# Optimization experiments

Measured on AMD Instinct MI355X. Metric: run time of the kernel, lower is better.

## Reference

```python
import jax, jax.numpy as jnp
import numpy as np
import math

EMB_DIM = 1024
NUM_HEADS = 16
D_H = EMB_DIM // NUM_HEADS
B, S = 2, 2048


def setup_inputs() -> dict:
    key = jax.random.key(0)
    ks = jax.random.split(key, 6)
    limit = math.sqrt(6.0 / (EMB_DIM + D_H))  # xavier_uniform per head
    x = jax.random.normal(ks[0], (B, S, EMB_DIM), dtype=jnp.float32)
    Wq = jax.random.uniform(ks[1], (NUM_HEADS, EMB_DIM, D_H), jnp.float32, -limit, limit)
    Wk = jax.random.uniform(ks[2], (NUM_HEADS, EMB_DIM, D_H), jnp.float32, -limit, limit)
    Wv = jax.random.uniform(ks[3], (NUM_HEADS, EMB_DIM, D_H), jnp.float32, -limit, limit)
    bq = jnp.zeros((NUM_HEADS, D_H), jnp.float32)
    bk = jnp.zeros((NUM_HEADS, D_H), jnp.float32)
    bv = jnp.zeros((NUM_HEADS, D_H), jnp.float32)
    limo = math.sqrt(6.0 / (EMB_DIM + EMB_DIM))
    W_O = jax.random.uniform(ks[4], (EMB_DIM, EMB_DIM), jnp.float32, -limo, limo)
    causal_mask = jnp.tril(jnp.ones((S, S), jnp.float32))
    padding_mask = jnp.zeros((B, S), jnp.bool_)  # all-False: nothing padded
    return {"x": x, "Wq": Wq, "bq": bq, "Wk": Wk, "bk": bk, "Wv": Wv,
            "bv": bv, "W_O": W_O, "causal_mask": causal_mask,
            "padding_mask": padding_mask}


def reference(x, Wq, bq, Wk, bk, Wv, bv, W_O, causal_mask, padding_mask):
    # Per-head projections, vectorized over heads: [B,S,E] x [H,E,D] -> [B,H,S,D]
    Q = jnp.einsum('bse,hed->bhsd', x, Wq) + bq[None, :, None, :]
    K = jnp.einsum('bse,hed->bhsd', x, Wk) + bk[None, :, None, :]
    V = jnp.einsum('bse,hed->bhsd', x, Wv) + bv[None, :, None, :]
    scores = jnp.einsum('bhsd,bhtd->bhst', Q, K) / math.sqrt(D_H)
    neg_inf = jnp.float32(-jnp.inf)
    scores = jnp.where(causal_mask[None, None, :, :] == 0, neg_inf, scores)
    scores = jnp.where(padding_mask[:, None, None, :], neg_inf, scores)
    attn = jax.nn.softmax(scores, axis=-1)
    out = jnp.einsum('bhst,bhtd->bhsd', attn, V)  # [B,H,S,D]
    # concat heads in order (dim=-1) -> [B,S,H*D]
    x_concat = out.transpose(0, 2, 1, 3).reshape(B, S, EMB_DIM)
    return x_concat @ W_O
```

## Files before the change

### kernel.cpp

```cpp
#include <hip/hip_runtime.h>
#include <hip/hip_bf16.h>


typedef __hip_bfloat16 bf16;
typedef __attribute__((ext_vector_type(8))) short bfrag;
typedef __attribute__((ext_vector_type(4))) float f32x4;
typedef __attribute__((ext_vector_type(16))) float f32x16;
typedef __attribute__((ext_vector_type(4))) short short4v;

#define MFMA16(a, b, c) __builtin_amdgcn_mfma_f32_16x16x32_bf16(a, b, c, 0, 0, 0)
#define MFMA32(a, b, c) __builtin_amdgcn_mfma_f32_32x32x16_bf16(a, b, c, 0, 0, 0)

__global__ __launch_bounds__(256) void prep_all(const float* __restrict__ x,
                                                const float* __restrict__ Wq,
                                                const float* __restrict__ Wk,
                                                const float* __restrict__ Wv,
                                                const float* __restrict__ Wo,
                                                bf16* __restrict__ xb,
                                                bf16* __restrict__ WqkvT,
                                                bf16* __restrict__ WoT) {
  __shared__ bf16 tile[64][80];
  int id = blockIdx.x;
  int t = threadIdx.x;
  if (id < 2048) {
    int i = id * 2048 + t * 8;
    float4 a = *(const float4*)(x + i);
    float4 b = *(const float4*)(x + i + 4);
    union { bf16 h[8]; bfrag v; } tmp;
    tmp.h[0] = __float2bfloat16(a.x); tmp.h[1] = __float2bfloat16(a.y);
    tmp.h[2] = __float2bfloat16(a.z); tmp.h[3] = __float2bfloat16(a.w);
    tmp.h[4] = __float2bfloat16(b.x); tmp.h[5] = __float2bfloat16(b.y);
    tmp.h[6] = __float2bfloat16(b.z); tmp.h[7] = __float2bfloat16(b.w);
    *(bfrag*)(xb + i) = tmp.v;
    return;
  }
  int wid = id - 2048;
  const float* src;
  bf16* dst;
  int srcld, dstld, r0, c0;
  if (wid < 768) {
    int w = wid >> 8, h = (wid >> 4) & 15;
    r0 = (wid & 15) * 64; c0 = 0;
    src = ((w == 0) ? Wq : (w == 1) ? Wk : Wv) + (long)h * 1024 * 64;
    dst = WqkvT + ((long)w * 1024 + h * 64) * 1024;
    srcld = 64; dstld = 1024;
  } else {
    int j = wid - 768;
    c0 = (j & 15) * 64; r0 = (j >> 4) * 64;
    src = Wo; dst = WoT;
    srcld = 1024; dstld = 1024;
  }
  int lr = t >> 3, lc = (t & 7) << 3;
#pragma unroll
  for (int p = 0; p < 2; ++p) {
    int r = lr + p * 32;
    const float* s = src + (long)(r0 + r) * srcld + c0 + lc;
    union { bf16 h8[8]; bfrag v; } tmp;
#pragma unroll
    for (int j = 0; j < 8; ++j) tmp.h8[j] = __float2bfloat16(s[j]);
    *(bfrag*)(&tile[r][lc]) = tmp.v;
  }
  __syncthreads();
#pragma unroll
  for (int p = 0; p < 2; ++p) {
    int c = lr + p * 32;
    union { bf16 h8[8]; bfrag v; } tmp;
#pragma unroll
    for (int j = 0; j < 8; ++j) tmp.h8[j] = tile[lc + j][c];
    *(bfrag*)(dst + (long)(c0 + c) * dstld + r0 + lc) = tmp.v;
  }
}

__global__ __launch_bounds__(256) void gemm_qkv128(const bf16* __restrict__ xb,
                                                   const bf16* __restrict__ WT,
                                                   const float* __restrict__ bq,
                                                   const float* __restrict__ bk,
                                                   const float* __restrict__ bv,
                                                   bf16* __restrict__ Q,
                                                   bf16* __restrict__ K_,
                                                   bf16* __restrict__ Vt) {
  const int K = 1024;
  __shared__ bf16 As[128][72];
  __shared__ bf16 Bs[128][72];
  int id = blockIdx.x;
  int xcd = id & 7, s = id >> 3;
  int m0 = ((xcd << 2) | (s & 3)) * 128;
  int n0 = (s >> 2) * 128;
  int t = threadIdx.x, wave = t >> 6, lane = t & 63, quad = lane >> 4, col = lane & 15;
  int wr = (wave >> 1) * 64, wc = (wave & 1) * 64;
  f32x4 acc[4][4] = {};

  int srow = t >> 1, scol = (t & 1) * 32;
  const bf16* Ag = xb + (long)(m0 + srow) * K + scol;
  const bf16* Bg = WT + (long)(n0 + srow) * K + scol;

  bfrag A0[4], B0[4], A1[4], B1[4];
#pragma unroll
  for (int i = 0; i < 4; ++i) {
    A0[i] = *(const bfrag*)(Ag + 8 * i);
    B0[i] = *(const bfrag*)(Bg + 8 * i);
    A1[i] = *(const bfrag*)(Ag + 64 + 8 * i);
    B1[i] = *(const bfrag*)(Bg + 64 + 8 * i);
  }

  for (int k0 = 0; k0 < K; k0 += 64) {
    __syncthreads();
#pragma unroll
    for (int i = 0; i < 4; ++i) {
      *(bfrag*)(&As[srow][scol + 8 * i]) = A0[i];
      *(bfrag*)(&Bs[srow][scol + 8 * i]) = B0[i];
    }
    int kn = (k0 + 128 < K) ? k0 + 128 : K - 64;
#pragma unroll
    for (int i = 0; i < 4; ++i) {
      A0[i] = A1[i]; B0[i] = B1[i];
      A1[i] = *(const bfrag*)(Ag + kn + 8 * i);
      B1[i] = *(const bfrag*)(Bg + kn + 8 * i);
    }
    __syncthreads();
#pragma unroll
    for (int kc = 0; kc < 2; ++kc) {
      bfrag ra[4], rb[4];
#pragma unroll
      for (int i = 0; i < 4; ++i)
        ra[i] = *(const bfrag*)(&As[wr + 16 * i + col][kc * 32 + quad * 8]);
#pragma unroll
      for (int c = 0; c < 4; ++c)
        rb[c] = *(const bfrag*)(&Bs[wc + 16 * c + col][kc * 32 + quad * 8]);
#pragma unroll
      for (int c = 0; c < 4; ++c)
#pragma unroll
        for (int i = 0; i < 4; ++i) acc[c][i] = MFMA16(ra[i], rb[c], acc[c][i]);
    }
  }

  int sel = n0 >> 10;
  const float* bias = (sel == 0) ? bq : (sel == 1) ? bk : bv;
#pragma unroll
  for (int c = 0; c < 4; ++c) {
    int nn = (n0 + wc + 16 * c + col) & 1023;
    float bvv = bias[nn];
    int h = nn >> 6, d = nn & 63;
#pragma unroll
    for (int i = 0; i < 4; ++i) {
      int mb = m0 + wr + 16 * i + quad * 4;
      int b = mb >> 11, s0 = mb & 2047;
      if (sel < 2) {
        bf16* dst = (sel == 0) ? Q : K_;
        long base = ((long)((b << 4) + h) * 2048 + s0) * 64 + d;
#pragma unroll
        for (int r = 0; r < 4; ++r)
          dst[base + (long)r * 64] = __float2bfloat16(acc[c][i][r] + bvv);
      } else {
        union { bf16 h4[4]; short4v v; } pk;
#pragma unroll
        for (int r = 0; r < 4; ++r) pk.h4[r] = __float2bfloat16(acc[c][i][r] + bvv);
        *(short4v*)(Vt + (long)(((b << 4) + h) * 64 + d) * 2048 + s0) = pk.v;
      }
    }
  }
}

__global__ __launch_bounds__(256) void gemm_out(const bf16* __restrict__ O,
                                                const bf16* __restrict__ Bt,
                                                float* __restrict__ Cf) {
  const int K = 1024;
  __shared__ bf16 As[128][72];
  __shared__ bf16 Bs[64][72];
  int id = blockIdx.x;
  int xcd = id & 7, s = id >> 3;
  int m0 = ((xcd << 2) | (s & 3)) * 128;
  int n0 = (s >> 2) * 64;
  int t = threadIdx.x;
  int wave = t >> 6, lane = t & 63, quad = lane >> 4, col = lane & 15;
  int wr = (wave >> 1) * 64, wc = (wave & 1) * 32;
  f32x4 acc[2][4] = {};

  int srA = t >> 1, scA = (t & 1) * 32;
  int srB = t >> 2, scB = (t & 3) * 16;
  int mrow = m0 + srA;
  int ob = mrow >> 11, os = mrow & 2047;
  const bf16* Ag = O + (long)ob * 2097152 + (long)os * 64 + scA;
  const bf16* Bg = Bt + (long)(n0 + srB) * K + scB;

  bfrag A0[4], A1[4];
  bfrag B0[2], B1[2];
#pragma unroll
  for (int i = 0; i < 4; ++i) {
    A0[i] = *(const bfrag*)(Ag + 8 * i);
    A1[i] = *(const bfrag*)(Ag + (long)64 * 2048 + 8 * i);
  }
#pragma unroll
  for (int i = 0; i < 2; ++i) {
    B0[i] = *(const bfrag*)(Bg + 8 * i);
    B1[i] = *(const bfrag*)(Bg + 64 + 8 * i);
  }

  for (int k0 = 0; k0 < K; k0 += 64) {
    __syncthreads();
#pragma unroll
    for (int i = 0; i < 4; ++i) *(bfrag*)(&As[srA][scA + 8 * i]) = A0[i];
#pragma unroll
    for (int i = 0; i < 2; ++i) *(bfrag*)(&Bs[srB][scB + 8 * i]) = B0[i];
    int kn = (k0 + 128 < K) ? k0 + 128 : K - 64;
#pragma unroll
    for (int i = 0; i < 4; ++i) {
      A0[i] = A1[i];
      A1[i] = *(const bfrag*)(Ag + (long)kn * 2048 + 8 * i);
    }
#pragma unroll
    for (int i = 0; i < 2; ++i) {
      B0[i] = B1[i];
      B1[i] = *(const bfrag*)(Bg + kn + 8 * i);
    }
    __syncthreads();
#pragma unroll
    for (int kc = 0; kc < 2; ++kc) {
      bfrag ra[4], rb[2];
#pragma unroll
      for (int i = 0; i < 4; ++i)
        ra[i] = *(const bfrag*)(&As[wr + 16 * i + col][kc * 32 + quad * 8]);
#pragma unroll
      for (int c = 0; c < 2; ++c)
        rb[c] = *(const bfrag*)(&Bs[wc + 16 * c + col][kc * 32 + quad * 8]);
#pragma unroll
      for (int c = 0; c < 2; ++c)
#pragma unroll
        for (int i = 0; i < 4; ++i) acc[c][i] = MFMA16(ra[i], rb[c], acc[c][i]);
    }
  }

#pragma unroll
  for (int c = 0; c < 2; ++c) {
    int n = n0 + wc + 16 * c + col;
#pragma unroll
    for (int i = 0; i < 4; ++i)
#pragma unroll
      for (int r = 0; r < 4; ++r) {
        int m = m0 + wr + 16 * i + quad * 4 + r;
        Cf[(long)m * 1024 + n] = acc[c][i][r];
      }
  }
}

__global__ __launch_bounds__(256) void attn_kernel(const bf16* __restrict__ Q,
                                                   const bf16* __restrict__ K_,
                                                   const bf16* __restrict__ Vt,
                                                   bf16* __restrict__ O) {
  int id = blockIdx.x;
  int xcd = id & 7, kk = id >> 3;
  int bh = ((kk & 3) << 3) | xcd;
  int pair = kk >> 2;

  __shared__ bf16 Ks[128][72];
  __shared__ bf16 Vs[64][136];
  __shared__ bf16 Ps[64][136];

  int t = threadIdx.x, wave = t >> 6, lane = t & 63;
  int qh = wave >> 1, jh = wave & 1, hi = lane >> 5, l5 = lane & 31;

  const float SC2 = 0.18033688f;

  int krow = t >> 3, kg = (t & 7) * 8;
  int vrow = t >> 4, vg = (t & 15) * 8;
  const bf16* Kbase = K_ + ((long)bh * 2048 + krow) * 64 + kg;
  const bf16* Vbase = Vt + ((long)bh * 64 + vrow) * 2048 + vg;

#pragma unroll
  for (int qsel = 0; qsel < 2; ++qsel) {
    int qt = qsel ? (31 - pair) : pair;
    int q0 = qt * 64;
    int nj = (qt >> 1) + 1;

    bfrag qa[4];
    const bf16* qp = Q + ((long)bh * 2048 + q0 + 32 * qh + l5) * 64 + hi * 8;
#pragma unroll
    for (int kd = 0; kd < 4; ++kd) qa[kd] = *(const bfrag*)(qp + kd * 16);

    f32x16 o0, o1;
    float lsum[16];
#pragma unroll
    for (int r = 0; r < 16; ++r) { o0[r] = 0.f; o1[r] = 0.f; lsum[r] = 0.f; }

    bfrag kreg[4], vreg[4];
#pragma unroll
    for (int i = 0; i < 4; ++i)
      kreg[i] = *(const bfrag*)(Kbase + (long)(32 * i) * 64);

    for (int jt = 0; jt < nj; ++jt) {
      int j0 = jt * 128;
      __syncthreads();
#pragma unroll
      for (int i = 0; i < 4; ++i)
        *(bfrag*)(&Ks[krow + 32 * i][kg]) = kreg[i];
      int jn = (jt + 1 < nj) ? (jt + 1) * 128 : jt * 128;
#pragma unroll
      for (int i = 0; i < 4; ++i)
        vreg[i] = *(const bfrag*)(Vbase + (long)(16 * i) * 2048 + j0);
#pragma unroll
      for (int i = 0; i < 4; ++i)
        kreg[i] = *(const bfrag*)(Kbase + (long)(jn + 32 * i) * 64);
      __syncthreads();

      f32x16 s0, s1;
#pragma unroll
      for (int r = 0; r < 16; ++r) { s0[r] = 0.f; s1[r] = 0.f; }
#pragma unroll
      for (int kd = 0; kd < 4; ++kd) {
        bfrag kb0 = *(const bfrag*)(&Ks[jh * 64 + l5][kd * 16 + hi * 8]);
        bfrag kb1 = *(const bfrag*)(&Ks[jh * 64 + 32 + l5][kd * 16 + hi * 8]);
        s0 = MFMA32(qa[kd], kb0, s0);
        s1 = MFMA32(qa[kd], kb1, s1);
      }

      bool lastT = (jt == nj - 1);
#pragma unroll
      for (int jb = 0; jb < 2; ++jb) {
        int j = j0 + jh * 64 + jb * 32 + l5;
#pragma unroll
        for (int r = 0; r < 16; ++r) {
          int qrow = (r & 3) + 8 * (r >> 2) + 4 * hi;
          float sv = jb ? s1[r] : s0[r];
          float p = __builtin_amdgcn_exp2f(fmaf(sv, SC2, -16.0f));
          if (lastT) p = (j <= q0 + 32 * qh + qrow) ? p : 0.f;
          lsum[r] += p;
          Ps[32 * qh + qrow][jh * 64 + jb * 32 + l5] = __float2bfloat16(p);
        }
      }
#pragma unroll
      for (int i = 0; i < 4; ++i)
        *(bfrag*)(&Vs[vrow + 16 * i][vg]) = vreg[i];
      __syncthreads();

#pragma unroll
      for (int kj = 0; kj < 4; ++kj) {
        bfrag pa = *(const bfrag*)(&Ps[32 * qh + l5][jh * 64 + kj * 16 + hi * 8]);
        bfrag vb0 = *(const bfrag*)(&Vs[l5][jh * 64 + kj * 16 + hi * 8]);
        bfrag vb1 = *(const bfrag*)(&Vs[32 + l5][jh * 64 + kj * 16 + hi * 8]);
        o0 = MFMA32(pa, vb0, o0);
        o1 = MFMA32(pa, vb1, o1);
      }
    }

#pragma unroll
    for (int off = 1; off < 32; off <<= 1)
#pragma unroll
      for (int r = 0; r < 16; ++r) lsum[r] += __shfl_xor(lsum[r], off, 64);

    __syncthreads();
    float* Osc = (float*)&Ps[0][0];
    float* Lsc = (float*)&Vs[0][0];
    if (jh == 1) {
#pragma unroll
      for (int r = 0; r < 16; ++r) {
        int qrow = (r & 3) + 8 * (r >> 2) + 4 * hi;
        Osc[(qh * 32 + qrow) * 68 + 0 * 32 + l5] = o0[r];
        Osc[(qh * 32 + qrow) * 68 + 1 * 32 + l5] = o1[r];
      }
      if (l5 == 0) {
#pragma unroll
        for (int r = 0; r < 16; ++r) {
          int qrow = (r & 3) + 8 * (r >> 2) + 4 * hi;
          Lsc[qh * 32 + qrow] = lsum[r];
        }
      }
    }
    __syncthreads();
    if (jh == 0) {
#pragma unroll
      for (int r = 0; r < 16; ++r) {
        int qrow = (r & 3) + 8 * (r >> 2) + 4 * hi;
        float inv = 1.f / (lsum[r] + Lsc[qh * 32 + qrow]);
        int iq = q0 + 32 * qh + qrow;
        float v0 = o0[r] + Osc[(qh * 32 + qrow) * 68 + 0 * 32 + l5];
        float v1 = o1[r] + Osc[(qh * 32 + qrow) * 68 + 1 * 32 + l5];
        O[((long)bh * 2048 + iq) * 64 + l5] = __float2bfloat16(v0 * inv);
        O[((long)bh * 2048 + iq) * 64 + 32 + l5] = __float2bfloat16(v1 * inv);
      }
    }
  }
}

extern "C" void kernel_launch(void* const* d_in, const int* in_sizes, int n_in,
                              void* d_out, int out_size, void* d_ws, size_t ws_size,
                              hipStream_t stream) {
  const float* x  = (const float*)d_in[0];
  const float* Wq = (const float*)d_in[1];
  const float* bq = (const float*)d_in[2];
  const float* Wk = (const float*)d_in[3];
  const float* bk = (const float*)d_in[4];
  const float* Wv = (const float*)d_in[5];
  const float* bv = (const float*)d_in[6];
  const float* Wo = (const float*)d_in[7];
  float* out = (float*)d_out;

  bf16* ws = (bf16*)d_ws;
  const long MB1 = 1 << 20;
  bf16* WqkvT = ws + 0 * MB1;
  bf16* WoT   = ws + 3 * MB1;
  bf16* Q     = ws + 4 * MB1;
  bf16* K_    = ws + 8 * MB1;
  bf16* Vt    = ws + 12 * MB1;
  bf16* O     = ws + 16 * MB1;
  bf16* xb    = ws + 20 * MB1;

  prep_all<<<3072, 256, 0, stream>>>(x, Wq, Wk, Wv, Wo, xb, WqkvT, WoT);
  gemm_qkv128<<<768, 256, 0, stream>>>(xb, WqkvT, bq, bk, bv, Q, K_, Vt);
  attn_kernel<<<512, 256, 0, stream>>>(Q, K_, Vt, O);
  gemm_out<<<512, 256, 0, stream>>>(O, WoT, out);
}
```

Measured before the change: 211.2 us.

## Stage GEMM epilogues through LDS for coalesced stores; split attention into per-tile blocks

The QKV and output GEMM epilogues now write accumulators into shared memory first and then store full 16-byte rows to global memory, replacing scattered 2-byte and 4-byte stores. The attention kernel no longer pairs a short and a long query tile inside each block. It launches 1024 blocks, one query tile each, ordered longest first. This is meant to cut uncoalesced write traffic and give the scheduler more, finer-grained work, at the cost of extra barriers and LDS round trips and less balanced per-block work.

```diff
diff --git a/kernel.cpp b/kernel.cpp
--- a/kernel.cpp
+++ b/kernel.cpp
@@ -80,12 +80,13 @@
                                                    bf16* __restrict__ K_,
                                                    bf16* __restrict__ Vt) {
   const int K = 1024;
-  __shared__ bf16 As[128][72];
-  __shared__ bf16 Bs[128][72];
+  __shared__ __align__(16) bf16 SH[2 * 128 * 72];
+#define AS(r, c) SH[(r) * 72 + (c)]
+#define BS(r, c) SH[9216 + (r) * 72 + (c)]
   int id = blockIdx.x;
-  int xcd = id & 7, s = id >> 3;
-  int m0 = ((xcd << 2) | (s & 3)) * 128;
-  int n0 = (s >> 2) * 128;
+  int xcd = id & 7, sw = id >> 3;
+  int m0 = ((xcd << 2) | (sw & 3)) * 128;
+  int n0 = (sw >> 2) * 128;
   int t = threadIdx.x, wave = t >> 6, lane = t & 63, quad = lane >> 4, col = lane & 15;
   int wr = (wave >> 1) * 64, wc = (wave & 1) * 64;
   f32x4 acc[4][4] = {};
@@ -107,8 +108,8 @@
     __syncthreads();
 #pragma unroll
     for (int i = 0; i < 4; ++i) {
-      *(bfrag*)(&As[srow][scol + 8 * i]) = A0[i];
-      *(bfrag*)(&Bs[srow][scol + 8 * i]) = B0[i];
+      *(bfrag*)(&AS(srow, scol + 8 * i)) = A0[i];
+      *(bfrag*)(&BS(srow, scol + 8 * i)) = B0[i];
     }
     int kn = (k0 + 128 < K) ? k0 + 128 : K - 64;
 #pragma unroll
@@ -123,10 +124,10 @@
       bfrag ra[4], rb[4];
 #pragma unroll
       for (int i = 0; i < 4; ++i)
-        ra[i] = *(const bfrag*)(&As[wr + 16 * i + col][kc * 32 + quad * 8]);
+        ra[i] = *(const bfrag*)(&AS(wr + 16 * i + col, kc * 32 + quad * 8));
 #pragma unroll
       for (int c = 0; c < 4; ++c)
-        rb[c] = *(const bfrag*)(&Bs[wc + 16 * c + col][kc * 32 + quad * 8]);
+        rb[c] = *(const bfrag*)(&BS(wc + 16 * c + col, kc * 32 + quad * 8));
 #pragma unroll
       for (int c = 0; c < 4; ++c)
 #pragma unroll
@@ -136,41 +137,68 @@
 
   int sel = n0 >> 10;
   const float* bias = (sel == 0) ? bq : (sel == 1) ? bk : bv;
-#pragma unroll
-  for (int c = 0; c < 4; ++c) {
-    int nn = (n0 + wc + 16 * c + col) & 1023;
-    float bvv = bias[nn];
-    int h = nn >> 6, d = nn & 63;
-#pragma unroll
-    for (int i = 0; i < 4; ++i) {
-      int mb = m0 + wr + 16 * i + quad * 4;
-      int b = mb >> 11, s0 = mb & 2047;
-      if (sel < 2) {
-        bf16* dst = (sel == 0) ? Q : K_;
-        long base = ((long)((b << 4) + h) * 2048 + s0) * 64 + d;
+  int blk_b = m0 >> 11, blk_s = m0 & 2047;
+  __syncthreads();
+
+  if (sel < 2) {
+#pragma unroll
+    for (int c = 0; c < 4; ++c) {
+      int nl = wc + 16 * c + col;
+      float bvv = bias[(n0 + nl) & 1023];
+#pragma unroll
+      for (int i = 0; i < 4; ++i) {
+        int mb = wr + 16 * i + quad * 4;
 #pragma unroll
         for (int r = 0; r < 4; ++r)
-          dst[base + (long)r * 64] = __float2bfloat16(acc[c][i][r] + bvv);
-      } else {
+          SH[(mb + r) * 136 + nl] = __float2bfloat16(acc[c][i][r] + bvv);
+      }
+    }
+    __syncthreads();
+    int m = t >> 1, half = t & 1;
+    int h = (((n0 & 1023) >> 6) + half);
+    bf16* dst = (sel == 0) ? Q : K_;
+    bf16* p = dst + (((long)(blk_b * 16 + h)) * 2048 + blk_s + m) * 64;
+#pragma unroll
+    for (int j = 0; j < 8; ++j)
+      *(bfrag*)(p + 8 * j) = *(const bfrag*)(&SH[m * 136 + half * 64 + 8 * j]);
+  } else {
+#pragma unroll
+    for (int c = 0; c < 4; ++c) {
+      int nl = wc + 16 * c + col;
+      float bvv = bias[(n0 + nl) & 1023];
+#pragma unroll
+      for (int i = 0; i < 4; ++i) {
+        int mb = wr + 16 * i + quad * 4;
         union { bf16 h4[4]; short4v v; } pk;
 #pragma unroll
         for (int r = 0; r < 4; ++r) pk.h4[r] = __float2bfloat16(acc[c][i][r] + bvv);
-        *(short4v*)(Vt + (long)(((b << 4) + h) * 64 + d) * 2048 + s0) = pk.v;
+        *(short4v*)(&SH[nl * 136 + mb]) = pk.v;
       }
     }
-  }
+    __syncthreads();
+    int nl = t >> 1, mhalf = (t & 1) * 64;
+    int h = ((n0 & 1023) + nl) >> 6, d = nl & 63;
+    bf16* p = Vt + ((long)(blk_b * 16 + h) * 64 + d) * 2048 + blk_s + mhalf;
+#pragma unroll
+    for (int j = 0; j < 8; ++j)
+      *(bfrag*)(p + 8 * j) = *(const bfrag*)(&SH[nl * 136 + mhalf + 8 * j]);
+  }
+#undef AS
+#undef BS
 }
 
 __global__ __launch_bounds__(256) void gemm_out(const bf16* __restrict__ O,
                                                 const bf16* __restrict__ Bt,
                                                 float* __restrict__ Cf) {
   const int K = 1024;
-  __shared__ bf16 As[128][72];
-  __shared__ bf16 Bs[64][72];
+  __shared__ __align__(16) char SHB[34816];
+  bf16* SH = (bf16*)SHB;
+#define AS(r, c) SH[(r) * 72 + (c)]
+#define BS(r, c) SH[9216 + (r) * 72 + (c)]
   int id = blockIdx.x;
-  int xcd = id & 7, s = id >> 3;
-  int m0 = ((xcd << 2) | (s & 3)) * 128;
-  int n0 = (s >> 2) * 64;
+  int xcd = id & 7, sw = id >> 3;
+  int m0 = ((xcd << 2) | (sw & 3)) * 128;
+  int n0 = (sw >> 2) * 64;
   int t = threadIdx.x;
   int wave = t >> 6, lane = t & 63, quad = lane >> 4, col = lane & 15;
   int wr = (wave >> 1) * 64, wc = (wave & 1) * 32;
@@ -199,9 +227,9 @@
   for (int k0 = 0; k0 < K; k0 += 64) {
     __syncthreads();
 #pragma unroll
-    for (int i = 0; i < 4; ++i) *(bfrag*)(&As[srA][scA + 8 * i]) = A0[i];
-#pragma unroll
-    for (int i = 0; i < 2; ++i) *(bfrag*)(&Bs[srB][scB + 8 * i]) = B0[i];
+    for (int i = 0; i < 4; ++i) *(bfrag*)(&AS(srA, scA + 8 * i)) = A0[i];
+#pragma unroll
+    for (int i = 0; i < 2; ++i) *(bfrag*)(&BS(srB, scB + 8 * i)) = B0[i];
     int kn = (k0 + 128 < K) ? k0 + 128 : K - 64;
 #pragma unroll
     for (int i = 0; i < 4; ++i) {
@@ -219,10 +247,10 @@
       bfrag ra[4], rb[2];
 #pragma unroll
       for (int i = 0; i < 4; ++i)
-        ra[i] = *(const bfrag*)(&As[wr + 16 * i + col][kc * 32 + quad * 8]);
+        ra[i] = *(const bfrag*)(&AS(wr + 16 * i + col, kc * 32 + quad * 8));
 #pragma unroll
       for (int c = 0; c < 2; ++c)
-        rb[c] = *(const bfrag*)(&Bs[wc + 16 * c + col][kc * 32 + quad * 8]);
+        rb[c] = *(const bfrag*)(&BS(wc + 16 * c + col, kc * 32 + quad * 8));
 #pragma unroll
       for (int c = 0; c < 2; ++c)
 #pragma unroll
@@ -230,17 +258,26 @@
     }
   }
 
+  __syncthreads();
+  float* T = (float*)SHB;
 #pragma unroll
   for (int c = 0; c < 2; ++c) {
-    int n = n0 + wc + 16 * c + col;
-#pragma unroll
-    for (int i = 0; i < 4; ++i)
-#pragma unroll
-      for (int r = 0; r < 4; ++r) {
-        int m = m0 + wr + 16 * i + quad * 4 + r;
-        Cf[(long)m * 1024 + n] = acc[c][i][r];
-      }
-  }
+    int nl = wc + 16 * c + col;
+#pragma unroll
+    for (int i = 0; i < 4; ++i) {
+      int mb = wr + 16 * i + quad * 4;
+#pragma unroll
+      for (int r = 0; r < 4; ++r) T[(mb + r) * 68 + nl] = acc[c][i][r];
+    }
+  }
+  __syncthreads();
+  int m = t >> 1, nhalf = (t & 1) * 32;
+  float* p = Cf + (long)(m0 + m) * 1024 + n0 + nhalf;
+#pragma unroll
+  for (int j = 0; j < 8; ++j)
+    *(float4*)(p + 4 * j) = *(const float4*)(&T[m * 68 + nhalf + 4 * j]);
+#undef AS
+#undef BS
 }
 
 __global__ __launch_bounds__(256) void attn_kernel(const bf16* __restrict__ Q,
@@ -248,9 +285,9 @@
                                                    const bf16* __restrict__ Vt,
                                                    bf16* __restrict__ O) {
   int id = blockIdx.x;
-  int xcd = id & 7, kk = id >> 3;
-  int bh = ((kk & 3) << 3) | xcd;
-  int pair = kk >> 2;
+  int xcd = id & 7, jj = id >> 3;
+  int qt = 31 - (jj >> 2);
+  int bh = ((jj & 3) << 3) | xcd;
 
   __shared__ bf16 Ks[128][72];
   __shared__ bf16 Vs[64][136];
@@ -266,117 +303,113 @@
   const bf16* Kbase = K_ + ((long)bh * 2048 + krow) * 64 + kg;
   const bf16* Vbase = Vt + ((long)bh * 64 + vrow) * 2048 + vg;
 
-#pragma unroll
-  for (int qsel = 0; qsel < 2; ++qsel) {
-    int qt = qsel ? (31 - pair) : pair;
-    int q0 = qt * 64;
-    int nj = (qt >> 1) + 1;
-
-    bfrag qa[4];
-    const bf16* qp = Q + ((long)bh * 2048 + q0 + 32 * qh + l5) * 64 + hi * 8;
-#pragma unroll
-    for (int kd = 0; kd < 4; ++kd) qa[kd] = *(const bfrag*)(qp + kd * 16);
-
-    f32x16 o0, o1;
-    float lsum[16];
-#pragma unroll
-    for (int r = 0; r < 16; ++r) { o0[r] = 0.f; o1[r] = 0.f; lsum[r] = 0.f; }
-
-    bfrag kreg[4], vreg[4];
+  int q0 = qt * 64;
+  int nj = (qt >> 1) + 1;
+
+  bfrag qa[4];
+  const bf16* qp = Q + ((long)bh * 2048 + q0 + 32 * qh + l5) * 64 + hi * 8;
+#pragma unroll
+  for (int kd = 0; kd < 4; ++kd) qa[kd] = *(const bfrag*)(qp + kd * 16);
+
+  f32x16 o0, o1;
+  float lsum[16];
+#pragma unroll
+  for (int r = 0; r < 16; ++r) { o0[r] = 0.f; o1[r] = 0.f; lsum[r] = 0.f; }
+
+  bfrag kreg[4], vreg[4];
+#pragma unroll
+  for (int i = 0; i < 4; ++i)
+    kreg[i] = *(const bfrag*)(Kbase + (long)(32 * i) * 64);
+
+  for (int jt = 0; jt < nj; ++jt) {
+    int j0 = jt * 128;
+    __syncthreads();
 #pragma unroll
     for (int i = 0; i < 4; ++i)
-      kreg[i] = *(const bfrag*)(Kbase + (long)(32 * i) * 64);
-
-    for (int jt = 0; jt < nj; ++jt) {
-      int j0 = jt * 128;
-      __syncthreads();
-#pragma unroll
-      for (int i = 0; i < 4; ++i)
-        *(bfrag*)(&Ks[krow + 32 * i][kg]) = kreg[i];
-      int jn = (jt + 1 < nj) ? (jt + 1) * 128 : jt * 128;
-#pragma unroll
-      for (int i = 0; i < 4; ++i)
-        vreg[i] = *(const bfrag*)(Vbase + (long)(16 * i) * 2048 + j0);
-#pragma unroll
-      for (int i = 0; i < 4; ++i)
-        kreg[i] = *(const bfrag*)(Kbase + (long)(jn + 32 * i) * 64);
-      __syncthreads();
-
-      f32x16 s0, s1;
-#pragma unroll
-      for (int r = 0; r < 16; ++r) { s0[r] = 0.f; s1[r] = 0.f; }
-#pragma unroll
-      for (int kd = 0; kd < 4; ++kd) {
-        bfrag kb0 = *(const bfrag*)(&Ks[jh * 64 + l5][kd * 16 + hi * 8]);
-        bfrag kb1 = *(const bfrag*)(&Ks[jh * 64 + 32 + l5][kd * 16 + hi * 8]);
-        s0 = MFMA32(qa[kd], kb0, s0);
-        s1 = MFMA32(qa[kd], kb1, s1);
-      }
-
-      bool lastT = (jt == nj - 1);
-#pragma unroll
-      for (int jb = 0; jb < 2; ++jb) {
-        int j = j0 + jh * 64 + jb * 32 + l5;
-#pragma unroll
-        for (int r = 0; r < 16; ++r) {
-          int qrow = (r & 3) + 8 * (r >> 2) + 4 * hi;
-          float sv = jb ? s1[r] : s0[r];
-          float p = __builtin_amdgcn_exp2f(fmaf(sv, SC2, -16.0f));
-          if (lastT) p = (j <= q0 + 32 * qh + qrow) ? p : 0.f;
-          lsum[r] += p;
-          Ps[32 * qh + qrow][jh * 64 + jb * 32 + l5] = __float2bfloat16(p);
-        }
-      }
-#pragma unroll
-      for (int i = 0; i < 4; ++i)
-        *(bfrag*)(&Vs[vrow + 16 * i][vg]) = vreg[i];
-      __syncthreads();
-
-#pragma unroll
-      for (int kj = 0; kj < 4; ++kj) {
-        bfrag pa = *(const bfrag*)(&Ps[32 * qh + l5][jh * 64 + kj * 16 + hi * 8]);
-        bfrag vb0 = *(const bfrag*)(&Vs[l5][jh * 64 + kj * 16 + hi * 8]);
-        bfrag vb1 = *(const bfrag*)(&Vs[32 + l5][jh * 64 + kj * 16 + hi * 8]);
-        o0 = MFMA32(pa, vb0, o0);
-        o1 = MFMA32(pa, vb1, o1);
-      }
-    }
-
-#pragma unroll
-    for (int off = 1; off < 32; off <<= 1)
-#pragma unroll
-      for (int r = 0; r < 16; ++r) lsum[r] += __shfl_xor(lsum[r], off, 64);
-
-    __syncthreads();
-    float* Osc = (float*)&Ps[0][0];
-    float* Lsc = (float*)&Vs[0][0];
-    if (jh == 1) {
+      *(bfrag*)(&Ks[krow + 32 * i][kg]) = kreg[i];
+    int jn = (jt + 1 < nj) ? (jt + 1) * 128 : jt * 128;
+#pragma unroll
+    for (int i = 0; i < 4; ++i)
+      vreg[i] = *(const bfrag*)(Vbase + (long)(16 * i) * 2048 + j0);
+#pragma unroll
+    for (int i = 0; i < 4; ++i)
+      kreg[i] = *(const bfrag*)(Kbase + (long)(jn + 32 * i) * 64);
+    __syncthreads();
+
+    f32x16 s0, s1;
+#pragma unroll
+    for (int r = 0; r < 16; ++r) { s0[r] = 0.f; s1[r] = 0.f; }
+#pragma unroll
+    for (int kd = 0; kd < 4; ++kd) {
+      bfrag kb0 = *(const bfrag*)(&Ks[jh * 64 + l5][kd * 16 + hi * 8]);
+      bfrag kb1 = *(const bfrag*)(&Ks[jh * 64 + 32 + l5][kd * 16 + hi * 8]);
+      s0 = MFMA32(qa[kd], kb0, s0);
+      s1 = MFMA32(qa[kd], kb1, s1);
+    }
+
+    bool lastT = (jt == nj - 1);
+#pragma unroll
+    for (int jb = 0; jb < 2; ++jb) {
+      int j = j0 + jh * 64 + jb * 32 + l5;
 #pragma unroll
       for (int r = 0; r < 16; ++r) {
         int qrow = (r & 3) + 8 * (r >> 2) + 4 * hi;
-        Osc[(qh * 32 + qrow) * 68 + 0 * 32 + l5] = o0[r];
-        Osc[(qh * 32 + qrow) * 68 + 1 * 32 + l5] = o1[r];
+        float sv = jb ? s1[r] : s0[r];
+        float p = __builtin_amdgcn_exp2f(fmaf(sv, SC2, -16.0f));
+        if (lastT) p = (j <= q0 + 32 * qh + qrow) ? p : 0.f;
+        lsum[r] += p;
+        Ps[32 * qh + qrow][jh * 64 + jb * 32 + l5] = __float2bfloat16(p);
       }
-      if (l5 == 0) {
-#pragma unroll
-        for (int r = 0; r < 16; ++r) {
-          int qrow = (r & 3) + 8 * (r >> 2) + 4 * hi;
-          Lsc[qh * 32 + qrow] = lsum[r];
-        }
-      }
-    }
-    __syncthreads();
-    if (jh == 0) {
+    }
+#pragma unroll
+    for (int i = 0; i < 4; ++i)
+      *(bfrag*)(&Vs[vrow + 16 * i][vg]) = vreg[i];
+    __syncthreads();
+
+#pragma unroll
+    for (int kj = 0; kj < 4; ++kj) {
+      bfrag pa = *(const bfrag*)(&Ps[32 * qh + l5][jh * 64 + kj * 16 + hi * 8]);
+      bfrag vb0 = *(const bfrag*)(&Vs[l5][jh * 64 + kj * 16 + hi * 8]);
+      bfrag vb1 = *(const bfrag*)(&Vs[32 + l5][jh * 64 + kj * 16 + hi * 8]);
+      o0 = MFMA32(pa, vb0, o0);
+      o1 = MFMA32(pa, vb1, o1);
+    }
+  }
+
+#pragma unroll
+  for (int off = 1; off < 32; off <<= 1)
+#pragma unroll
+    for (int r = 0; r < 16; ++r) lsum[r] += __shfl_xor(lsum[r], off, 64);
+
+  __syncthreads();
+  float* Osc = (float*)&Ps[0][0];
+  float* Lsc = (float*)&Vs[0][0];
+  if (jh == 1) {
+#pragma unroll
+    for (int r = 0; r < 16; ++r) {
+      int qrow = (r & 3) + 8 * (r >> 2) + 4 * hi;
+      Osc[(qh * 32 + qrow) * 68 + 0 * 32 + l5] = o0[r];
+      Osc[(qh * 32 + qrow) * 68 + 1 * 32 + l5] = o1[r];
+    }
+    if (l5 == 0) {
 #pragma unroll
       for (int r = 0; r < 16; ++r) {
         int qrow = (r & 3) + 8 * (r >> 2) + 4 * hi;
-        float inv = 1.f / (lsum[r] + Lsc[qh * 32 + qrow]);
-        int iq = q0 + 32 * qh + qrow;
-        float v0 = o0[r] + Osc[(qh * 32 + qrow) * 68 + 0 * 32 + l5];
-        float v1 = o1[r] + Osc[(qh * 32 + qrow) * 68 + 1 * 32 + l5];
-        O[((long)bh * 2048 + iq) * 64 + l5] = __float2bfloat16(v0 * inv);
-        O[((long)bh * 2048 + iq) * 64 + 32 + l5] = __float2bfloat16(v1 * inv);
+        Lsc[qh * 32 + qrow] = lsum[r];
       }
+    }
+  }
+  __syncthreads();
+  if (jh == 0) {
+#pragma unroll
+    for (int r = 0; r < 16; ++r) {
+      int qrow = (r & 3) + 8 * (r >> 2) + 4 * hi;
+      float inv = 1.f / (lsum[r] + Lsc[qh * 32 + qrow]);
+      int iq = q0 + 32 * qh + qrow;
+      float v0 = o0[r] + Osc[(qh * 32 + qrow) * 68 + 0 * 32 + l5];
+      float v1 = o1[r] + Osc[(qh * 32 + qrow) * 68 + 1 * 32 + l5];
+      O[((long)bh * 2048 + iq) * 64 + l5] = __float2bfloat16(v0 * inv);
+      O[((long)bh * 2048 + iq) * 64 + 32 + l5] = __float2bfloat16(v1 * inv);
     }
   }
 }
@@ -406,6 +439,6 @@
 
   prep_all<<<3072, 256, 0, stream>>>(x, Wq, Wk, Wv, Wo, xb, WqkvT, WoT);
   gemm_qkv128<<<768, 256, 0, stream>>>(xb, WqkvT, bq, bk, bv, Q, K_, Vt);
-  attn_kernel<<<512, 256, 0, stream>>>(Q, K_, Vt, O);
+  attn_kernel<<<1024, 256, 0, stream>>>(Q, K_, Vt, O);
   gemm_out<<<512, 256, 0, stream>>>(O, WoT, out);
 }
```

After: 218.2 us. +3.3%, slower.

## Keep attention probabilities in registers via transposed MFMA and split query tiles per block

Applied to the files above, without the earlier changes.

The attention kernel now computes S^T = K·Q^T so each lane holds probabilities for a single query row. The P tile is packed to bf16 and exchanged across half-waves with shuffles to form the PV MFMA operand, removing the Ps shared-memory round trip and the 16-way row-sum reductions. Each block now handles one query tile instead of a paired short/long tile, with the grid doubled and heaviest tiles scheduled first. Output is staged through LDS for coalesced 16-byte stores. The cost is uneven per-block work that depends on hardware scheduling to balance, plus extra shuffle traffic.

```diff
diff --git a/kernel.cpp b/kernel.cpp
--- a/kernel.cpp
+++ b/kernel.cpp
@@ -10,6 +10,13 @@
 
 #define MFMA16(a, b, c) __builtin_amdgcn_mfma_f32_16x16x32_bf16(a, b, c, 0, 0, 0)
 #define MFMA32(a, b, c) __builtin_amdgcn_mfma_f32_32x32x16_bf16(a, b, c, 0, 0, 0)
+
+__device__ __forceinline__ unsigned pkbf(float a, float b) {
+  union { bf16 h[2]; unsigned u; } w;
+  w.h[0] = __float2bfloat16(a);
+  w.h[1] = __float2bfloat16(b);
+  return w.u;
+}
 
 __global__ __launch_bounds__(256) void prep_all(const float* __restrict__ x,
                                                 const float* __restrict__ Wq,
@@ -83,9 +90,9 @@
   __shared__ bf16 As[128][72];
   __shared__ bf16 Bs[128][72];
   int id = blockIdx.x;
-  int xcd = id & 7, s = id >> 3;
-  int m0 = ((xcd << 2) | (s & 3)) * 128;
-  int n0 = (s >> 2) * 128;
+  int xcd = id & 7, sw = id >> 3;
+  int m0 = ((xcd << 2) | (sw & 3)) * 128;
+  int n0 = (sw >> 2) * 128;
   int t = threadIdx.x, wave = t >> 6, lane = t & 63, quad = lane >> 4, col = lane & 15;
   int wr = (wave >> 1) * 64, wc = (wave & 1) * 64;
   f32x4 acc[4][4] = {};
@@ -168,9 +175,9 @@
   __shared__ bf16 As[128][72];
   __shared__ bf16 Bs[64][72];
   int id = blockIdx.x;
-  int xcd = id & 7, s = id >> 3;
-  int m0 = ((xcd << 2) | (s & 3)) * 128;
-  int n0 = (s >> 2) * 64;
+  int xcd = id & 7, sw = id >> 3;
+  int m0 = ((xcd << 2) | (sw & 3)) * 128;
+  int n0 = (sw >> 2) * 64;
   int t = threadIdx.x;
   int wave = t >> 6, lane = t & 63, quad = lane >> 4, col = lane & 15;
   int wr = (wave >> 1) * 64, wc = (wave & 1) * 32;
@@ -248,13 +255,12 @@
                                                    const bf16* __restrict__ Vt,
                                                    bf16* __restrict__ O) {
   int id = blockIdx.x;
-  int xcd = id & 7, kk = id >> 3;
-  int bh = ((kk & 3) << 3) | xcd;
-  int pair = kk >> 2;
+  int xcd = id & 7, jj = id >> 3;
+  int qt = 31 - (jj >> 2);
+  int bh = ((jj & 3) << 3) | xcd;
 
   __shared__ bf16 Ks[128][72];
   __shared__ bf16 Vs[64][136];
-  __shared__ bf16 Ps[64][136];
 
   int t = threadIdx.x, wave = t >> 6, lane = t & 63;
   int qh = wave >> 1, jh = wave & 1, hi = lane >> 5, l5 = lane & 31;
@@ -266,119 +272,132 @@
   const bf16* Kbase = K_ + ((long)bh * 2048 + krow) * 64 + kg;
   const bf16* Vbase = Vt + ((long)bh * 64 + vrow) * 2048 + vg;
 
-#pragma unroll
-  for (int qsel = 0; qsel < 2; ++qsel) {
-    int qt = qsel ? (31 - pair) : pair;
-    int q0 = qt * 64;
-    int nj = (qt >> 1) + 1;
-
-    bfrag qa[4];
-    const bf16* qp = Q + ((long)bh * 2048 + q0 + 32 * qh + l5) * 64 + hi * 8;
-#pragma unroll
-    for (int kd = 0; kd < 4; ++kd) qa[kd] = *(const bfrag*)(qp + kd * 16);
-
-    f32x16 o0, o1;
-    float lsum[16];
-#pragma unroll
-    for (int r = 0; r < 16; ++r) { o0[r] = 0.f; o1[r] = 0.f; lsum[r] = 0.f; }
-
-    bfrag kreg[4], vreg[4];
+  int q0 = qt * 64;
+  int nj = (qt >> 1) + 1;
+  int qi = q0 + 32 * qh + l5;
+
+  bfrag qa[4];
+  const bf16* qp = Q + ((long)bh * 2048 + q0 + 32 * qh + l5) * 64 + hi * 8;
+#pragma unroll
+  for (int kd = 0; kd < 4; ++kd) qa[kd] = *(const bfrag*)(qp + kd * 16);
+
+  f32x16 o0, o1;
+  float lsum = 0.f;
+#pragma unroll
+  for (int r = 0; r < 16; ++r) { o0[r] = 0.f; o1[r] = 0.f; }
+
+  bfrag kreg[4], vreg[4];
+#pragma unroll
+  for (int i = 0; i < 4; ++i)
+    kreg[i] = *(const bfrag*)(Kbase + (long)(32 * i) * 64);
+
+  for (int jt = 0; jt < nj; ++jt) {
+    int j0 = jt * 128;
+    __syncthreads();
 #pragma unroll
     for (int i = 0; i < 4; ++i)
-      kreg[i] = *(const bfrag*)(Kbase + (long)(32 * i) * 64);
-
-    for (int jt = 0; jt < nj; ++jt) {
-      int j0 = jt * 128;
-      __syncthreads();
-#pragma unroll
-      for (int i = 0; i < 4; ++i)
-        *(bfrag*)(&Ks[krow + 32 * i][kg]) = kreg[i];
-      int jn = (jt + 1 < nj) ? (jt + 1) * 128 : jt * 128;
-#pragma unroll
-      for (int i = 0; i < 4; ++i)
-        vreg[i] = *(const bfrag*)(Vbase + (long)(16 * i) * 2048 + j0);
-#pragma unroll
-      for (int i = 0; i < 4; ++i)
-        kreg[i] = *(const bfrag*)(Kbase + (long)(jn + 32 * i) * 64);
-      __syncthreads();
-
-      f32x16 s0, s1;
-#pragma unroll
-      for (int r = 0; r < 16; ++r) { s0[r] = 0.f; s1[r] = 0.f; }
-#pragma unroll
-      for (int kd = 0; kd < 4; ++kd) {
-        bfrag kb0 = *(const bfrag*)(&Ks[jh * 64 + l5][kd * 16 + hi * 8]);
-        bfrag kb1 = *(const bfrag*)(&Ks[jh * 64 + 32 + l5][kd * 16 + hi * 8]);
-        s0 = MFMA32(qa[kd], kb0, s0);
-        s1 = MFMA32(qa[kd], kb1, s1);
+      *(bfrag*)(&Ks[krow + 32 * i][kg]) = kreg[i];
+    int jn = (jt + 1 < nj) ? (jt + 1) * 128 : jt * 128;
+#pragma unroll
+    for (int i = 0; i < 4; ++i)
+      vreg[i] = *(const bfrag*)(Vbase + (long)(16 * i) * 2048 + j0);
+#pragma unroll
+    for (int i = 0; i < 4; ++i)
+      kreg[i] = *(const bfrag*)(Kbase + (long)(jn + 32 * i) * 64);
+    __syncthreads();
+
+    f32x16 s0, s1;
+#pragma unroll
+    for (int r = 0; r < 16; ++r) { s0[r] = 0.f; s1[r] = 0.f; }
+#pragma unroll
+    for (int kd = 0; kd < 4; ++kd) {
+      bfrag ka0 = *(const bfrag*)(&Ks[jh * 64 + l5][kd * 16 + hi * 8]);
+      bfrag ka1 = *(const bfrag*)(&Ks[jh * 64 + 32 + l5][kd * 16 + hi * 8]);
+      s0 = MFMA32(ka0, qa[kd], s0);
+      s1 = MFMA32(ka1, qa[kd], s1);
+    }
+
+    bool lastT = (jt == nj - 1);
+    unsigned g[2][4][2];
+#pragma unroll
+    for (int jb = 0; jb < 2; ++jb) {
+      float pv[16];
+#pragma unroll
+      for (int r = 0; r < 16; ++r) {
+        int jl = (r & 3) + 8 * (r >> 2) + 4 * hi;
+        int j = j0 + jh * 64 + jb * 32 + jl;
+        float sv = jb ? s1[r] : s0[r];
+        float p = __builtin_amdgcn_exp2f(fmaf(sv, SC2, -16.0f));
+        if (lastT) p = (j <= qi) ? p : 0.f;
+        lsum += p;
+        pv[r] = p;
       }
-
-      bool lastT = (jt == nj - 1);
-#pragma unroll
-      for (int jb = 0; jb < 2; ++jb) {
-        int j = j0 + jh * 64 + jb * 32 + l5;
-#pragma unroll
-        for (int r = 0; r < 16; ++r) {
-          int qrow = (r & 3) + 8 * (r >> 2) + 4 * hi;
-          float sv = jb ? s1[r] : s0[r];
-          float p = __builtin_amdgcn_exp2f(fmaf(sv, SC2, -16.0f));
-          if (lastT) p = (j <= q0 + 32 * qh + qrow) ? p : 0.f;
-          lsum[r] += p;
-          Ps[32 * qh + qrow][jh * 64 + jb * 32 + l5] = __float2bfloat16(p);
-        }
+#pragma unroll
+      for (int gg = 0; gg < 4; ++gg) {
+        g[jb][gg][0] = pkbf(pv[4 * gg], pv[4 * gg + 1]);
+        g[jb][gg][1] = pkbf(pv[4 * gg + 2], pv[4 * gg + 3]);
       }
-#pragma unroll
-      for (int i = 0; i < 4; ++i)
-        *(bfrag*)(&Vs[vrow + 16 * i][vg]) = vreg[i];
-      __syncthreads();
-
-#pragma unroll
-      for (int kj = 0; kj < 4; ++kj) {
-        bfrag pa = *(const bfrag*)(&Ps[32 * qh + l5][jh * 64 + kj * 16 + hi * 8]);
-        bfrag vb0 = *(const bfrag*)(&Vs[l5][jh * 64 + kj * 16 + hi * 8]);
-        bfrag vb1 = *(const bfrag*)(&Vs[32 + l5][jh * 64 + kj * 16 + hi * 8]);
-        o0 = MFMA32(pa, vb0, o0);
-        o1 = MFMA32(pa, vb1, o1);
+    }
+#pragma unroll
+    for (int i = 0; i < 4; ++i)
+      *(bfrag*)(&Vs[vrow + 16 * i][vg]) = vreg[i];
+    __syncthreads();
+
+#pragma unroll
+    for (int jb = 0; jb < 2; ++jb) {
+#pragma unroll
+      for (int c = 0; c < 2; ++c) {
+        unsigned a0 = g[jb][2 * c][0], a1 = g[jb][2 * c][1];
+        unsigned b0 = g[jb][2 * c + 1][0], b1 = g[jb][2 * c + 1][1];
+        unsigned sa0 = __shfl_xor((int)a0, 32, 64);
+        unsigned sa1 = __shfl_xor((int)a1, 32, 64);
+        unsigned sb0 = __shfl_xor((int)b0, 32, 64);
+        unsigned sb1 = __shfl_xor((int)b1, 32, 64);
+        union { unsigned u[4]; bfrag f; } pf;
+        pf.u[0] = hi ? sb0 : a0;
+        pf.u[1] = hi ? sb1 : a1;
+        pf.u[2] = hi ? b0 : sa0;
+        pf.u[3] = hi ? b1 : sa1;
+        int kk = jh * 64 + jb * 32 + c * 16 + hi * 8;
+        bfrag av0 = *(const bfrag*)(&Vs[l5][kk]);
+        bfrag av1 = *(const bfrag*)(&Vs[32 + l5][kk]);
+        o0 = MFMA32(av0, pf.f, o0);
+        o1 = MFMA32(av1, pf.f, o1);
       }
     }
-
-#pragma unroll
-    for (int off = 1; off < 32; off <<= 1)
-#pragma unroll
-      for (int r = 0; r < 16; ++r) lsum[r] += __shfl_xor(lsum[r], off, 64);
-
-    __syncthreads();
-    float* Osc = (float*)&Ps[0][0];
-    float* Lsc = (float*)&Vs[0][0];
-    if (jh == 1) {
-#pragma unroll
-      for (int r = 0; r < 16; ++r) {
-        int qrow = (r & 3) + 8 * (r >> 2) + 4 * hi;
-        Osc[(qh * 32 + qrow) * 68 + 0 * 32 + l5] = o0[r];
-        Osc[(qh * 32 + qrow) * 68 + 1 * 32 + l5] = o1[r];
-      }
-      if (l5 == 0) {
-#pragma unroll
-        for (int r = 0; r < 16; ++r) {
-          int qrow = (r & 3) + 8 * (r >> 2) + 4 * hi;
-          Lsc[qh * 32 + qrow] = lsum[r];
-        }
-      }
-    }
-    __syncthreads();
-    if (jh == 0) {
-#pragma unroll
-      for (int r = 0; r < 16; ++r) {
-        int qrow = (r & 3) + 8 * (r >> 2) + 4 * hi;
-        float inv = 1.f / (lsum[r] + Lsc[qh * 32 + qrow]);
-        int iq = q0 + 32 * qh + qrow;
-        float v0 = o0[r] + Osc[(qh * 32 + qrow) * 68 + 0 * 32 + l5];
-        float v1 = o1[r] + Osc[(qh * 32 + qrow) * 68 + 1 * 32 + l5];
-        O[((long)bh * 2048 + iq) * 64 + l5] = __float2bfloat16(v0 * inv);
-        O[((long)bh * 2048 + iq) * 64 + 32 + l5] = __float2bfloat16(v1 * inv);
-      }
-    }
-  }
+  }
+
+  lsum += __shfl_xor(lsum, 32, 64);
+
+  __syncthreads();
+  float* Osc = (float*)&Ks[0][0];
+  float* Lsc = (float*)&Vs[0][0];
+  bf16* Of = (bf16*)((char*)&Vs[0][0] + 512);
+  int q = 32 * qh + l5;
+  if (jh == 1) {
+#pragma unroll
+    for (int r = 0; r < 16; ++r) {
+      int d = (r & 3) + 8 * (r >> 2) + 4 * hi;
+      Osc[q * 68 + d] = o0[r];
+      Osc[q * 68 + 32 + d] = o1[r];
+    }
+    if (hi == 0) Lsc[q] = lsum;
+  }
+  __syncthreads();
+  if (jh == 0) {
+    float inv = 1.f / (lsum + Lsc[q]);
+#pragma unroll
+    for (int r = 0; r < 16; ++r) {
+      int d = (r & 3) + 8 * (r >> 2) + 4 * hi;
+      Of[q * 72 + d] = __float2bfloat16((o0[r] + Osc[q * 68 + d]) * inv);
+      Of[q * 72 + 32 + d] = __float2bfloat16((o1[r] + Osc[q * 68 + 32 + d]) * inv);
+    }
+  }
+  __syncthreads();
+  int row = t >> 2, off = (t & 3) * 16;
+  bf16* po = O + ((long)bh * 2048 + q0 + row) * 64 + off;
+  *(bfrag*)(po) = *(const bfrag*)(&Of[row * 72 + off]);
+  *(bfrag*)(po + 8) = *(const bfrag*)(&Of[row * 72 + off + 8]);
 }
 
 extern "C" void kernel_launch(void* const* d_in, const int* in_sizes, int n_in,
@@ -406,6 +425,6 @@
 
   prep_all<<<3072, 256, 0, stream>>>(x, Wq, Wk, Wv, Wo, xb, WqkvT, WoT);
   gemm_qkv128<<<768, 256, 0, stream>>>(xb, WqkvT, bq, bk, bv, Q, K_, Vt);
-  attn_kernel<<<512, 256, 0, stream>>>(Q, K_, Vt, O);
+  attn_kernel<<<1024, 256, 0, stream>>>(Q, K_, Vt, O);
   gemm_out<<<512, 256, 0, stream>>>(O, WoT, out);
 }
```

After: 202.3 us. 1.04x faster.
